# Optimization experiments

Hardware: AMD Instinct MI355X
Metric: run time of the kernel (lower is better)

Reference implementation:

```python
import jax, jax.numpy as jnp
import numpy as np

B, T, C, H = 2, 2048, 1024, 16
HD = C // H  # 64
KSZ = 3      # conv kernel size; causal left-pad = KSZ - 1


def _causal_dwconv(x, w, b):
    """Depthwise causal conv1d. x: (B,T,Ch), w: (Ch,KSZ), b: (Ch,) -> (B,T,Ch)."""
    xc = jnp.transpose(x, (0, 2, 1))                      # (B,Ch,T)
    xp = jnp.pad(xc, ((0, 0), (0, 0), (KSZ - 1, 0)))      # left pad only -> causal
    kern = w[:, None, :]                                  # (O=Ch, I=1, W=KSZ)
    y = jax.lax.conv_general_dilated(
        xp, kern, window_strides=(1,), padding='VALID',
        feature_group_count=xc.shape[1],
        dimension_numbers=('NCW', 'OIW', 'NCW'))          # (B,Ch,T)
    y = y + b[None, :, None]
    return jnp.transpose(y, (0, 2, 1))                    # (B,T,Ch)


def setup_inputs() -> dict:
    key = jax.random.key(0)
    ks = jax.random.split(key, 9)
    s = 0.02
    return {
        'x':        jax.random.normal(ks[0], (B, T, C), jnp.float32),
        'Wqkv':     jax.random.normal(ks[1], (C + 2 * HD, C), jnp.float32) * s,
        'q_conv_w': jax.random.normal(ks[2], (C, KSZ), jnp.float32) * s,
        'q_conv_b': jax.random.normal(ks[3], (C,), jnp.float32) * s,
        'k_conv_w': jax.random.normal(ks[4], (HD, KSZ), jnp.float32) * s,
        'k_conv_b': jax.random.normal(ks[5], (HD,), jnp.float32) * s,
        'v_conv_w': jax.random.normal(ks[6], (HD, KSZ), jnp.float32) * s,
        'v_conv_b': jax.random.normal(ks[7], (HD,), jnp.float32) * s,
        'Wproj':    jax.random.normal(ks[8], (C, C), jnp.float32) * s,
    }


def reference(x, Wqkv, q_conv_w, q_conv_b, k_conv_w, k_conv_b,
              v_conv_w, v_conv_b, Wproj):
    # fused QKV projection (no bias; config.bias=False)
    qkv = jnp.einsum('btc,oc->bto', x, Wqkv)              # (B,T,C+2*HD)
    q = qkv[..., :C]                                      # (B,T,C)
    k = qkv[..., C:C + HD]                                # (B,T,HD)
    v = qkv[..., C + HD:]                                 # (B,T,HD)

    # depthwise causal convs
    q = _causal_dwconv(q, q_conv_w, q_conv_b)
    k = _causal_dwconv(k, k_conv_w, k_conv_b)
    v = _causal_dwconv(v, v_conv_w, v_conv_b)

    # multi-query attention: H query heads, 1 shared k/v head
    qh = q.reshape(B, T, H, HD).transpose(0, 2, 1, 3)     # (B,H,T,HD)
    scale = 1.0 / np.sqrt(HD).astype(np.float32)
    scores = jnp.einsum('bhqd,bkd->bhqk', qh, k) * scale  # (B,H,T,T)
    causal = jnp.tril(jnp.ones((T, T), bool))
    scores = jnp.where(causal[None, None], scores, jnp.finfo(scores.dtype).min)
    attn = jax.nn.softmax(scores, axis=-1)
    y = jnp.einsum('bhqk,bkd->bhqd', attn, v)             # (B,H,T,HD)
    y = y.transpose(0, 2, 1, 3).reshape(B, T, C)          # (B,T,C)
    return jnp.einsum('btc,oc->bto', y, Wproj)            # output proj
```

## Files before the change

### kernel.cpp

```cpp
#include <hip/hip_runtime.h>
#include <hip/hip_bf16.h>

#define B_ 2
#define T_ 2048
#define C_ 1024
#define H_ 16
#define HD_ 64
#define O_ 1152

#define NX  (B_ * T_ * C_)
#define NW1 (O_ * C_)
#define NW2 (C_ * C_)

#define QSCALE 0.1803368801111244f

typedef __attribute__((ext_vector_type(8))) short bf16x8;
typedef __attribute__((ext_vector_type(4))) float f32x4;
typedef __attribute__((ext_vector_type(16))) float f32x16;
typedef __attribute__((ext_vector_type(4))) unsigned u32x4;
typedef __attribute__((ext_vector_type(2))) unsigned u32x2;

__device__ inline short f2bf(float f) {
    union { float f; unsigned u; } v; v.f = f;
    unsigned r = v.u + 0x7FFFu + ((v.u >> 16) & 1u);
    return (short)(r >> 16);
}
__device__ inline float bf2f(short s) {
    union { unsigned u; float f; } v; v.u = ((unsigned)(unsigned short)s) << 16;
    return v.f;
}
__device__ inline float exp2fast(float x) { return __builtin_amdgcn_exp2f(x); }
__device__ inline unsigned cvtpk(float lo, float hi) {
    unsigned r;
    asm("v_cvt_pk_bf16_f32 %0, %1, %2" : "=v"(r) : "v"(lo), "v"(hi));
    return r;
}
__device__ inline u32x2 pswap(unsigned a, unsigned b) {
    return __builtin_amdgcn_permlane32_swap(a, b, false, false);
}
__device__ inline float xmax32(float x) {
    u32x2 r = pswap(__float_as_uint(x), __float_as_uint(x));
    return fmaxf(__uint_as_float(r[0]), __uint_as_float(r[1]));
}
__device__ inline float xadd32(float x) {
    u32x2 r = pswap(__float_as_uint(x), __float_as_uint(x));
    return __uint_as_float(r[0]) + __uint_as_float(r[1]);
}

#define GLL16(gp, lp) __builtin_amdgcn_global_load_lds( \
    (const __attribute__((address_space(1))) unsigned int*)(gp), \
    (__attribute__((address_space(3))) unsigned int*)(lp), 16, 0, 0)

__global__ __launch_bounds__(256) void cvt_bf16(const float* __restrict__ x,
        const float* __restrict__ w1, const float* __restrict__ w2,
        short* __restrict__ xb, short* __restrict__ w1b, short* __restrict__ w2b) {
    size_t i = ((size_t)blockIdx.x * 256 + threadIdx.x) * 8;
    const float* src; short* dst; size_t off;
    if (i < (size_t)NX)              { src = x;  dst = xb;  off = i; }
    else if (i < (size_t)NX + NW1)   { src = w1; dst = w1b; off = i - NX; }
    else                             { src = w2; dst = w2b; off = i - NX - NW1; }
    f32x4 a = *(const f32x4*)(src + off);
    f32x4 b = *(const f32x4*)(src + off + 4);
    bf16x8 r;
    r[0] = f2bf(a[0]); r[1] = f2bf(a[1]); r[2] = f2bf(a[2]); r[3] = f2bf(a[3]);
    r[4] = f2bf(b[0]); r[5] = f2bf(b[1]); r[6] = f2bf(b[2]); r[7] = f2bf(b[3]);
    *(bf16x8*)(dst + off) = r;
}

template <bool OUT_BF16>
__global__ __launch_bounds__(256) void gemm_bt(const short* __restrict__ A,
                                               const short* __restrict__ Bm,
                                               void* __restrict__ Cv,
                                               int M, int N, int K) {
    __shared__ short lA[2][128 * 32];
    __shared__ short lB[2][64 * 32];
    int ntn = N >> 6;
    int nwg = (M >> 7) * ntn;
    int cpx = nwg >> 3;
    int bid = (int)blockIdx.x;
    int swz = (bid % 8) * cpx + bid / 8;
    int m0 = (swz / ntn) << 7;
    int n0 = (swz % ntn) << 6;
    int t = threadIdx.x;
    int wid = t >> 6, l = t & 63;
    int wr = wid >> 1, wc = wid & 1;
    int c = l & 15, g = l >> 4;

    const short* gA0 = A + (size_t)(m0 + (t >> 2)) * K + (t & 3) * 8;
    const short* gA1 = gA0 + (size_t)64 * K;
    const short* gB0 = Bm + (size_t)(n0 + (t >> 2)) * K + (t & 3) * 8;

    int nstep = K >> 5;
    f32x4 acc[4][2] = {};
    int cur = 0;
    GLL16(gA0, &lA[0][t * 8]);
    GLL16(gA1, &lA[0][64 * 32 + t * 8]);
    GLL16(gB0, &lB[0][t * 8]);
    for (int it = 0; it < nstep; it++) {
        __syncthreads();
        if (it + 1 < nstep) {
            int k = (it + 1) << 5;
            GLL16(gA0 + k, &lA[cur ^ 1][t * 8]);
            GLL16(gA1 + k, &lA[cur ^ 1][64 * 32 + t * 8]);
            GLL16(gB0 + k, &lB[cur ^ 1][t * 8]);
        }
        const short* lap = &lA[cur][(wr * 64 + c) * 32 + g * 8];
        const short* lbp = &lB[cur][(wc * 32 + c) * 32 + g * 8];
        bf16x8 a[4], b[2];
        #pragma unroll
        for (int i = 0; i < 4; i++) a[i] = *(const bf16x8*)(lap + i * 16 * 32);
        #pragma unroll
        for (int j = 0; j < 2; j++) b[j] = *(const bf16x8*)(lbp + j * 16 * 32);
        #pragma unroll
        for (int i = 0; i < 4; i++)
            #pragma unroll
            for (int j = 0; j < 2; j++)
                acc[i][j] = __builtin_amdgcn_mfma_f32_16x16x32_bf16(a[i], b[j], acc[i][j], 0, 0, 0);
        cur ^= 1;
    }

    #pragma unroll
    for (int i = 0; i < 4; i++)
        #pragma unroll
        for (int j = 0; j < 2; j++)
            #pragma unroll
            for (int r = 0; r < 4; r++) {
                int rr = m0 + wr * 64 + i * 16 + g * 4 + r;
                int cc = n0 + wc * 32 + j * 16 + c;
                if (OUT_BF16)
                    ((short*)Cv)[(size_t)rr * N + cc] = f2bf(acc[i][j][r]);
                else
                    ((float*)Cv)[(size_t)rr * N + cc] = acc[i][j][r];
            }
}

__global__ __launch_bounds__(256) void conv_split(const short* __restrict__ qkv,
        const float* __restrict__ qw, const float* __restrict__ qb,
        const float* __restrict__ kw, const float* __restrict__ kbias,
        const float* __restrict__ vw, const float* __restrict__ vbias,
        short* __restrict__ Qs, short* __restrict__ Kb, short* __restrict__ Vt) {
    int idx = blockIdx.x * 256 + threadIdx.x;
    int ch = idx % O_;
    int bt = idx / O_;
    int t = bt % T_;
    int b = bt / T_;
    const short* p = qkv + (size_t)bt * O_ + ch;
    float x2 = bf2f(p[0]);
    float x1 = (t >= 1) ? bf2f(p[-O_]) : 0.f;
    float x0 = (t >= 2) ? bf2f(p[-2 * O_]) : 0.f;
    float w0, w1, w2, bias;
    if (ch < C_)             { w0 = qw[ch*3]; w1 = qw[ch*3+1]; w2 = qw[ch*3+2]; bias = qb[ch]; }
    else if (ch < C_ + HD_)  { int cc = ch - C_;       w0 = kw[cc*3]; w1 = kw[cc*3+1]; w2 = kw[cc*3+2]; bias = kbias[cc]; }
    else                     { int cc = ch - C_ - HD_; w0 = vw[cc*3]; w1 = vw[cc*3+1]; w2 = vw[cc*3+2]; bias = vbias[cc]; }
    float y = fmaf(x0, w0, fmaf(x1, w1, fmaf(x2, w2, bias)));
    if (ch < C_) {
        int h = ch >> 6, d = ch & 63;
        Qs[(((size_t)b * H_ + h) * T_ + t) * HD_ + d] = f2bf(y * QSCALE);
    } else if (ch < C_ + HD_) {
        Kb[((size_t)b * T_ + t) * HD_ + (ch - C_)] = f2bf(y);
    } else {
        Vt[((size_t)b * HD_ + (ch - C_ - HD_)) * T_ + t] = f2bf(y);
    }
}

__global__ __launch_bounds__(256, 2) void attn_kernel(const short* __restrict__ Qs,
        const short* __restrict__ Kb, const short* __restrict__ Vt,
        short* __restrict__ Y) {
    __shared__ short KL[2][2][64 * 64];
    __shared__ short VL[2][2][64 * 64];
    int n = (int)blockIdx.x;
    int half = n >> 8;
    int n2 = n & 255;
    int y = n2 >> 5;
    int qx = n2 & 31;
    int qt = half ? qx : 63 - qx;
    int b = y >> 2;
    int hq = y & 3;
    int t = threadIdx.x;
    int wid = t >> 6, l = t & 63;
    int ql = l & 31, hi = l >> 5;
    int h = hq * 4 + wid;
    int bh = b * H_ + h;
    int qbase = qt * 32;
    int qi = qbase + ql;

    const short* Qp = Qs + ((size_t)bh * T_ + qi) * HD_ + hi * 8;
    bf16x8 qf[4];
    #pragma unroll
    for (int s = 0; s < 4; s++) qf[s] = *(const bf16x8*)(Qp + s * 16);

    f32x16 Oa0 = {}, Oa1 = {};
    float mrow = -1e30f, lsum = 0.f;

    const short* Kbase = Kb + (size_t)b * T_ * HD_;
    const short* Vbase = Vt + (size_t)b * HD_ * T_;

    int krow = t >> 3;
    int sc = ((t & 7) ^ (krow & 7)) * 8;
    const short* KgA = Kbase + (size_t)krow * HD_ + sc;
    const short* VgA = Vbase + (size_t)krow * T_ + sc;
    int t8 = t * 8;

    auto STAGE1 = [&](short* Kd, short* Vd, int kt0) {
        GLL16(KgA + (size_t)kt0 * HD_, Kd + t8);
        GLL16(KgA + (size_t)(kt0 + 32) * HD_, Kd + 2048 + t8);
        GLL16(VgA + kt0, Vd + t8);
        GLL16(VgA + kt0 + (size_t)32 * T_, Vd + 2048 + t8);
    };

    auto PROC = [&](const short* Kt, const short* Vtl, int kt0) {
        f32x16 sv0 = {}, sv1 = {};
        #pragma unroll
        for (int s = 0; s < 4; s++) {
            bf16x8 ka = *(const bf16x8*)&Kt[ql * 64 + (((s * 2 + hi) ^ (ql & 7)) * 8)];
            sv0 = __builtin_amdgcn_mfma_f32_32x32x16_bf16(ka, qf[s], sv0, 0, 0, 0);
        }
        #pragma unroll
        for (int s = 0; s < 4; s++) {
            bf16x8 ka = *(const bf16x8*)&Kt[(32 + ql) * 64 + (((s * 2 + hi) ^ (ql & 7)) * 8)];
            sv1 = __builtin_amdgcn_mfma_f32_32x32x16_bf16(ka, qf[s], sv1, 0, 0, 0);
        }
        if (kt0 + 64 > qbase) {
            #pragma unroll
            for (int r = 0; r < 16; r++) {
                int kl = (r & 3) + 8 * (r >> 2) + 4 * hi;
                if (kt0 + kl > qi)      sv0[r] = -1e30f;
                if (kt0 + 32 + kl > qi) sv1[r] = -1e30f;
            }
        }
        float t8v[8];
        #pragma unroll
        for (int r = 0; r < 8; r++)
            t8v[r] = fmaxf(fmaxf(sv0[r], sv0[r + 8]), fmaxf(sv1[r], sv1[r + 8]));
        float pmax = fmaxf(fmaxf(fmaxf(t8v[0], t8v[4]), fmaxf(t8v[1], t8v[5])),
                           fmaxf(fmaxf(t8v[2], t8v[6]), fmaxf(t8v[3], t8v[7])));
        pmax = xmax32(pmax);
        if (!__all(pmax <= mrow + 8.f)) {
            float nm = fmaxf(mrow, pmax);
            float alpha = exp2fast(mrow - nm);
            mrow = nm;
            lsum *= alpha;
            #pragma unroll
            for (int r = 0; r < 16; r++) { Oa0[r] *= alpha; Oa1[r] *= alpha; }
        }
        #pragma unroll
        for (int r = 0; r < 16; r++) sv0[r] = exp2fast(sv0[r] - mrow);
        #pragma unroll
        for (int r = 0; r < 16; r++) sv1[r] = exp2fast(sv1[r] - mrow);
        float s8[8];
        #pragma unroll
        for (int r = 0; r < 8; r++)
            s8[r] = (sv0[r] + sv0[r + 8]) + (sv1[r] + sv1[r + 8]);
        float psum = ((s8[0] + s8[4]) + (s8[1] + s8[5])) +
                     ((s8[2] + s8[6]) + (s8[3] + s8[7]));
        lsum += xadd32(psum);
        #pragma unroll
        for (int sub = 0; sub < 2; sub++) {
            #pragma unroll
            for (int hh = 0; hh < 2; hh++) {
                unsigned X0, X1, X2, X3;
                if (sub == 0) {
                    X0 = cvtpk(sv0[hh * 8 + 0], sv0[hh * 8 + 1]);
                    X1 = cvtpk(sv0[hh * 8 + 2], sv0[hh * 8 + 3]);
                    X2 = cvtpk(sv0[hh * 8 + 4], sv0[hh * 8 + 5]);
                    X3 = cvtpk(sv0[hh * 8 + 6], sv0[hh * 8 + 7]);
                } else {
                    X0 = cvtpk(sv1[hh * 8 + 0], sv1[hh * 8 + 1]);
                    X1 = cvtpk(sv1[hh * 8 + 2], sv1[hh * 8 + 3]);
                    X2 = cvtpk(sv1[hh * 8 + 4], sv1[hh * 8 + 5]);
                    X3 = cvtpk(sv1[hh * 8 + 6], sv1[hh * 8 + 7]);
                }
                u32x2 r02 = pswap(X0, X2);
                u32x2 r13 = pswap(X1, X3);
                union { u32x4 u; bf16x8 v; } pw;
                pw.u[0] = r02[0];
                pw.u[1] = r13[0];
                pw.u[2] = r02[1];
                pw.u[3] = r13[1];
                int u = sub * 2 + hh;
                bf16x8 va0 = *(const bf16x8*)&Vtl[ql * 64 + (((u * 2 + hi) ^ (ql & 7)) * 8)];
                bf16x8 va1 = *(const bf16x8*)&Vtl[(32 + ql) * 64 + (((u * 2 + hi) ^ (ql & 7)) * 8)];
                Oa0 = __builtin_amdgcn_mfma_f32_32x32x16_bf16(va0, pw.v, Oa0, 0, 0, 0);
                Oa1 = __builtin_amdgcn_mfma_f32_32x32x16_bf16(va1, pw.v, Oa1, 0, 0, 0);
            }
        }
    };

    int nt = (qt >> 1) + 1;
    int nr = (nt + 1) >> 1;
    int cur = 0;
    STAGE1(KL[0][0], VL[0][0], 0);
    STAGE1(KL[0][1], VL[0][1], 64);
    for (int r = 0; r < nr; r++) {
        __syncthreads();
        if (r + 1 < nr) {
            int base = (r + 1) * 128;
            STAGE1(KL[cur ^ 1][0], VL[cur ^ 1][0], base);
            STAGE1(KL[cur ^ 1][1], VL[cur ^ 1][1], base + 64);
        }
        PROC(KL[cur][0], VL[cur][0], r * 128);
        if (r * 2 + 1 < nt)
            PROC(KL[cur][1], VL[cur][1], r * 128 + 64);
        cur ^= 1;
    }
    float inv = 1.f / lsum;
    size_t orow = ((size_t)b * T_ + qi) * C_ + h * HD_;
    #pragma unroll
    for (int r = 0; r < 16; r += 2) {
        int d = (r & 3) + 8 * (r >> 2) + 4 * hi;
        *(unsigned*)(Y + orow + d)      = cvtpk(Oa0[r] * inv, Oa0[r + 1] * inv);
        *(unsigned*)(Y + orow + 32 + d) = cvtpk(Oa1[r] * inv, Oa1[r + 1] * inv);
    }
}

extern "C" void kernel_launch(void* const* d_in, const int* in_sizes, int n_in,
                              void* d_out, int out_size, void* d_ws, size_t ws_size,
                              hipStream_t stream) {
    const float* x     = (const float*)d_in[0];
    const float* Wqkv  = (const float*)d_in[1];
    const float* qw    = (const float*)d_in[2];
    const float* qb    = (const float*)d_in[3];
    const float* kw    = (const float*)d_in[4];
    const float* kbias = (const float*)d_in[5];
    const float* vw    = (const float*)d_in[6];
    const float* vbias = (const float*)d_in[7];
    const float* Wproj = (const float*)d_in[8];

    char* ws = (char*)d_ws;
    short* xb     = (short*)ws;
    short* Wqkvb  = (short*)(ws + 8388608);
    short* Wprojb = (short*)(ws + 10747904);
    short* qkvb   = (short*)(ws + 12845056);
    short* Qsc    = (short*)(ws + 22282240);
    short* Kbf    = (short*)(ws + 30670848);
    short* Vtr    = (short*)(ws + 31195136);
    short* Ybf    = xb;

    const int M = B_ * T_;

    cvt_bf16<<<dim3(3136), 256, 0, stream>>>(x, Wqkv, Wproj, xb, Wqkvb, Wprojb);

    gemm_bt<true><<<dim3((M / 128) * (O_ / 64)), 256, 0, stream>>>(
        xb, Wqkvb, qkvb, M, O_, C_);

    conv_split<<<dim3((B_ * T_ * O_) / 256), 256, 0, stream>>>(
        qkvb, qw, qb, kw, kbias, vw, vbias, Qsc, Kbf, Vtr);

    attn_kernel<<<dim3(512), 256, 0, stream>>>(Qsc, Kbf, Vtr, Ybf);

    gemm_bt<false><<<dim3((M / 128) * (C_ / 64)), 256, 0, stream>>>(
        Ybf, Wprojb, (float*)d_out, M, C_, C_);
}
```

Before: 108.7 us.

## Double GEMM K-tile to 64 with XOR-swizzled LDS layout

The GEMM main loop now stages 64-wide K slices instead of 32, which halves the number of barrier/prefetch iterations per tile. The global-to-LDS loads permute 16-byte chunks with an XOR of the row index, and the fragment reads undo the same permutation to cut LDS bank conflicts. This doubles LDS usage per block (48KB), which may reduce occupancy.

```diff
diff --git a/kernel.cpp b/kernel.cpp
--- a/kernel.cpp
+++ b/kernel.cpp
@@ -72,8 +72,8 @@
                                                const short* __restrict__ Bm,
                                                void* __restrict__ Cv,
                                                int M, int N, int K) {
-    __shared__ short lA[2][128 * 32];
-    __shared__ short lB[2][64 * 32];
+    __shared__ short lA[2][128 * 64];
+    __shared__ short lB[2][64 * 64];
     int ntn = N >> 6;
     int nwg = (M >> 7) * ntn;
     int cpx = nwg >> 3;
@@ -86,36 +86,60 @@
     int wr = wid >> 1, wc = wid & 1;
     int c = l & 15, g = l >> 4;
 
-    const short* gA0 = A + (size_t)(m0 + (t >> 2)) * K + (t & 3) * 8;
-    const short* gA1 = gA0 + (size_t)64 * K;
-    const short* gB0 = Bm + (size_t)(n0 + (t >> 2)) * K + (t & 3) * 8;
-
-    int nstep = K >> 5;
+    const short* gAsrc[4];
+    int lAoff[4];
+    #pragma unroll
+    for (int i = 0; i < 4; i++) {
+        int cidx = t + i * 256;
+        int row = cidx >> 3, sl = cidx & 7;
+        gAsrc[i] = A + (size_t)(m0 + row) * K + ((sl ^ (row & 7)) * 8);
+        lAoff[i] = cidx * 8;
+    }
+    const short* gBsrc[2];
+    int lBoff[2];
+    #pragma unroll
+    for (int i = 0; i < 2; i++) {
+        int cidx = t + i * 256;
+        int row = cidx >> 3, sl = cidx & 7;
+        gBsrc[i] = Bm + (size_t)(n0 + row) * K + ((sl ^ (row & 7)) * 8);
+        lBoff[i] = cidx * 8;
+    }
+
+    int nstep = K >> 6;
     f32x4 acc[4][2] = {};
     int cur = 0;
-    GLL16(gA0, &lA[0][t * 8]);
-    GLL16(gA1, &lA[0][64 * 32 + t * 8]);
-    GLL16(gB0, &lB[0][t * 8]);
+    #pragma unroll
+    for (int i = 0; i < 4; i++) GLL16(gAsrc[i], &lA[0][lAoff[i]]);
+    #pragma unroll
+    for (int i = 0; i < 2; i++) GLL16(gBsrc[i], &lB[0][lBoff[i]]);
     for (int it = 0; it < nstep; it++) {
         __syncthreads();
         if (it + 1 < nstep) {
-            int k = (it + 1) << 5;
-            GLL16(gA0 + k, &lA[cur ^ 1][t * 8]);
-            GLL16(gA1 + k, &lA[cur ^ 1][64 * 32 + t * 8]);
-            GLL16(gB0 + k, &lB[cur ^ 1][t * 8]);
-        }
-        const short* lap = &lA[cur][(wr * 64 + c) * 32 + g * 8];
-        const short* lbp = &lB[cur][(wc * 32 + c) * 32 + g * 8];
-        bf16x8 a[4], b[2];
-        #pragma unroll
-        for (int i = 0; i < 4; i++) a[i] = *(const bf16x8*)(lap + i * 16 * 32);
-        #pragma unroll
-        for (int j = 0; j < 2; j++) b[j] = *(const bf16x8*)(lbp + j * 16 * 32);
-        #pragma unroll
-        for (int i = 0; i < 4; i++)
-            #pragma unroll
-            for (int j = 0; j < 2; j++)
-                acc[i][j] = __builtin_amdgcn_mfma_f32_16x16x32_bf16(a[i], b[j], acc[i][j], 0, 0, 0);
+            int k = (it + 1) << 6;
+            #pragma unroll
+            for (int i = 0; i < 4; i++) GLL16(gAsrc[i] + k, &lA[cur ^ 1][lAoff[i]]);
+            #pragma unroll
+            for (int i = 0; i < 2; i++) GLL16(gBsrc[i] + k, &lB[cur ^ 1][lBoff[i]]);
+        }
+        #pragma unroll
+        for (int ks = 0; ks < 2; ks++) {
+            bf16x8 a[4], b[2];
+            #pragma unroll
+            for (int i = 0; i < 4; i++) {
+                int row = wr * 64 + i * 16 + c;
+                a[i] = *(const bf16x8*)&lA[cur][row * 64 + (((ks * 4 + g) ^ (row & 7)) * 8)];
+            }
+            #pragma unroll
+            for (int j = 0; j < 2; j++) {
+                int row = wc * 32 + j * 16 + c;
+                b[j] = *(const bf16x8*)&lB[cur][row * 64 + (((ks * 4 + g) ^ (row & 7)) * 8)];
+            }
+            #pragma unroll
+            for (int i = 0; i < 4; i++)
+                #pragma unroll
+                for (int j = 0; j < 2; j++)
+                    acc[i][j] = __builtin_amdgcn_mfma_f32_16x16x32_bf16(a[i], b[j], acc[i][j], 0, 0, 0);
+        }
         cur ^= 1;
     }
 
```

After: 99.48 us. 8.4% less time.
